# Kernel optimization log

Hardware: AMD Instinct MI355X
Metric: run time of the kernel (lower is better)

The kernel has to match this reference:

```python
import jax, jax.numpy as jnp
import numpy as np
from jax import lax

B, D, S, H, W, T = 128, 512, 30, 14, 14, 12


def setup_inputs() -> dict:
    key = jax.random.key(0)
    ks = jax.random.split(key, 28)
    f = lambda k, shape: jax.random.normal(k, shape, jnp.float32) * 0.05
    return {
        "q": f(ks[0], (B, D)),
        "cws": f(ks[1], (B, D, S)),
        "KB": f(ks[2], (B, D, H, W)),
        "c0": f(ks[3], (B, D)),
        "m0": f(ks[4], (B, D)),
        "Wq": f(ks[5], (D, D)), "bq": f(ks[6], (D,)),
        "Wct": f(ks[7], (2 * D, D)), "bct": f(ks[8], (D,)),
        "wca": f(ks[9], (D,)), "bca": f(ks[10], ()),
        "Wm": f(ks[11], (D, D)), "bm": f(ks[12], (D,)),
        "Wkb": f(ks[13], (D, D)), "bkb": f(ks[14], (D,)),
        "Wrm": f(ks[15], (2 * D, D)), "brm": f(ks[16], (D,)),
        "wra": f(ks[17], (D,)), "bra": f(ks[18], ()),
        "Wwm": f(ks[19], (2 * D, D)), "bwm": f(ks[20], (D,)),
        "wwa": f(ks[21], (D,)), "bwa": f(ks[22], ()),
        "Wam": f(ks[23], (2 * D, D)), "bam": f(ks[24], (D,)),
        "Wg": f(ks[25], (D, D)), "bg": f(ks[26], (D,)),
        "steps": T,
    }


def _mac(q, cws, KB, c0, m0, Wq, bq, Wct, bct, wca, bca, Wm, bm, Wkb, bkb,
         Wrm, brm, wra, bra, Wwm, bwm, wwa, bwa, Wam, bam, Wg, bg, steps):
    b, d, h, w = KB.shape[0], KB.shape[1], KB.shape[2], KB.shape[3]
    KBp = jnp.transpose(KB, (0, 2, 3, 1))          # B,H,W,d
    KB2 = KBp @ Wkb + bkb                           # KB_transform (step-invariant)
    q_i = q @ Wq + bq                               # q_transform (step-invariant)

    nhist = steps + 1
    c_hist = jnp.zeros((nhist, b, d), KB.dtype).at[0].set(c0)
    m_hist = jnp.zeros((nhist, b, d), KB.dtype).at[0].set(m0)

    def step(carry, t):
        c_hist, m_hist, c_prev, m_prev = carry
        # ---- ControlUnit ----
        cq = jnp.concatenate([q_i, c_prev], axis=-1) @ Wct + bct   # B,d
        clog = jnp.einsum('bds,d->bs', cq[:, :, None] * cws, wca) + bca
        cattn = jax.nn.softmax(clog, axis=-1)                       # B,S
        c_i = jnp.einsum('bs,bds->bd', cattn, cws)
        # ---- ReadUnit ----
        mp = m_prev @ Wm + bm                                       # B,d
        I = mp[:, None, None, :] * KB2                              # B,H,W,d
        Im = jnp.concatenate([I, KBp], axis=-1) @ Wrm + brm         # B,H,W,d
        rlog = jnp.einsum('bhwd,d->bhw', c_i[:, None, None, :] * Im, wra) + bra
        rattn = jax.nn.softmax(rlog.reshape(b, -1), axis=-1).reshape(b, h, w)
        m_new = jnp.einsum('bhw,bhwd->bd', rattn, KBp)
        # ---- WriteUnit (self_attn + mem_gate) ----
        _m = jnp.concatenate([m_new, m_prev], axis=-1) @ Wwm + bwm
        slog = jnp.einsum('tbd,d->bt', c_i[None] * c_hist, wwa) + bwa
        valid = jnp.arange(nhist) <= t
        slog = jnp.where(valid[None, :], slog, jnp.float32(-1e9))
        sattn = jax.nn.softmax(slog, axis=-1)                       # B,T+1
        m_sa = jnp.einsum('bt,tbd->bd', sattn, m_hist)
        _m = jnp.concatenate([m_sa, _m], axis=-1) @ Wam + bam
        g = jax.nn.sigmoid(c_i @ Wg + bg)
        _m = g * m_prev + (1.0 - g) * _m
        c_hist = c_hist.at[t + 1].set(c_i)
        m_hist = m_hist.at[t + 1].set(_m)
        return (c_hist, m_hist, c_i, _m), None

    (c_hist, m_hist, c_last, m_last), _ = lax.scan(
        step, (c_hist, m_hist, c0, m0), jnp.arange(steps))
    return m_last


def reference(q, cws, KB, c0, m0, Wq, bq, Wct, bct, wca, bca, Wm, bm, Wkb, bkb,
              Wrm, brm, wra, bra, Wwm, bwm, wwa, bwa, Wam, bam, Wg, bg, steps):
    return _mac(q, cws, KB, c0, m0, Wq, bq, Wct, bct, wca, bca, Wm, bm, Wkb, bkb,
                Wrm, brm, wra, bra, Wwm, bwm, wwa, bwa, Wam, bam, Wg, bg, steps)
```

## Files before the change

kernel.cpp:

```cpp
#include <hip/hip_runtime.h>
#include <cstdint>

#define BB 128
#define DD 512
#define SS 30
#define PP 196
#define TT 12
#define BD (BB*DD)

typedef unsigned short ushortT;
typedef unsigned int uintT;

__device__ __forceinline__ float bf2f(ushortT u)
{
    return __uint_as_float(((uintT)u) << 16);
}
__device__ __forceinline__ ushortT f2bf(float f)
{
    uintT b = __float_as_uint(f);
    return (ushortT)((b + 0x7FFFu + ((b >> 16) & 1u)) >> 16);
}

struct GDesc {
    const float *A0, *A1;
    const ushortT *W0, *W1;
    const float *bias;
    float *out;
    const float *e1;
    int nparts, epi, mblk, nblk, aux;
};
struct GPack { GDesc d[6]; };

__global__ __launch_bounds__(256)
void gemm4(GPack pk)
{
    GDesc d = pk.d[blockIdx.z];
    if ((int)blockIdx.x >= d.mblk || (int)blockIdx.y >= d.nblk) return;
    const int tid  = threadIdx.x;
    const int lane = tid & 63;
    const int wv   = __builtin_amdgcn_readfirstlane(tid >> 6);

    if (d.epi == 5) {
        int bb = (blockIdx.x * 4 + blockIdx.y) * 2;
        #pragma unroll
        for (int b = bb; b < bb + 2; ++b) {
            const float* sat = d.e1 + b * 16;
            float a0 = 0.f, a1 = 0.f;
            for (int tp = 0; tp <= d.aux; ++tp) {
                float s = sat[tp];
                const float* mh = d.A0 + (size_t)tp * BD + (size_t)b * DD;
                a0 = fmaf(s, mh[tid], a0);
                a1 = fmaf(s, mh[tid + 256], a1);
            }
            d.out[(size_t)b * DD + tid] = a0;
            d.out[(size_t)b * DD + tid + 256] = a1;
        }
        return;
    }

    const int m0 = blockIdx.x * 8;
    const int c0 = blockIdx.y * 128;
    float accx[8], accy[8];
    #pragma unroll
    for (int m = 0; m < 8; ++m) { accx[m] = 0.f; accy[m] = 0.f; }

    for (int p = 0; p < d.nparts; ++p) {
        const float* A = p ? d.A1 : d.A0;
        const ushortT* W = p ? d.W1 : d.W0;
        const float* a = A + (size_t)m0 * 512 + wv * 128;
        const uintT* Wb = (const uintT*)(W + (size_t)(wv * 128) * 512 + c0) + lane;
        #pragma unroll 4
        for (int k = 0; k < 128; ++k) {
            uintT w = Wb[(size_t)k * 256];
            float wx = __uint_as_float(w << 16);
            float wy = __uint_as_float(w & 0xFFFF0000u);
            #pragma unroll
            for (int m = 0; m < 8; ++m) {
                float av = a[m * 512 + k];
                accx[m] = fmaf(av, wx, accx[m]);
                accy[m] = fmaf(av, wy, accy[m]);
            }
        }
    }

    __shared__ float red[4][8][128];
    #pragma unroll
    for (int m = 0; m < 8; ++m)
        *(float2*)&red[wv][m][lane * 2] = make_float2(accx[m], accy[m]);
    __syncthreads();

    for (int i = tid; i < 1024; i += 256) {
        int mm = i >> 7, cl = i & 127;
        float s = (red[0][mm][cl] + red[1][mm][cl])
                + (red[2][mm][cl] + red[3][mm][cl]);
        int row = m0 + mm, col = c0 + cl;
        size_t o = (size_t)row * 512 + col;
        if (d.epi == 0)      d.out[o] = s + d.bias[col];
        else if (d.epi == 1) { float v = s + d.bias[col];
                               d.out[o] = 1.f / (1.f + __expf(-v)); }
        else if (d.epi == 4) d.out[o] = s + d.e1[o];
        else if (d.epi == 7) ((ushortT*)d.out)[o] = f2bf(s);
        else                 d.out[o] = s;
    }
}

struct SP {
    const float *cq, *cws, *wca, *bca, *wra, *wwa, *bwa;
    const ushortT *cwsTh;
    float *c_hist, *sattn, *vb;
    const float *msa, *mnw, *gb, *b2;
    const ushortT *WamH, *WAH, *WBH;
    float *m_hist, *dst;
    int t;
};

__global__ __launch_bounds__(512)
void stepA(SP P)
{
    const int tid = threadIdx.x;
    const int lane = tid & 63;
    __shared__ float cqw[512], ciw[512];
    __shared__ float clog2[32], cattn[32], slog[16];
    __shared__ float red[8][2][128];

    if ((int)blockIdx.x < 128) {
        if (P.t >= TT) return;
        int b = blockIdx.x, w = tid >> 6, t = P.t;
        cqw[tid] = P.cq[(size_t)b*DD + tid] * P.wca[tid];
        __syncthreads();
        for (int s = w; s < SS; s += 8) {
            const ushortT* row = P.cwsTh + ((size_t)b*SS + s)*DD;
            float a = 0.f;
            #pragma unroll
            for (int j = 0; j < 8; ++j)
                a = fmaf(cqw[lane + 64*j], bf2f(row[lane + 64*j]), a);
            for (int off = 32; off; off >>= 1) a += __shfl_xor(a, off, 64);
            if (lane == 0) clog2[s] = a;
        }
        __syncthreads();
        if (tid < 32) {
            float v = (tid < SS) ? clog2[tid] + P.bca[0] : -1e30f;
            float mx = v;
            for (int off = 16; off; off >>= 1) mx = fmaxf(mx, __shfl_xor(mx, off, 32));
            float e = (tid < SS) ? __expf(v - mx) : 0.f;
            float sm = e;
            for (int off = 16; off; off >>= 1) sm += __shfl_xor(sm, off, 32);
            cattn[tid] = e / sm;
        }
        __syncthreads();
        {
            const float* base = P.cws + (size_t)b*DD*SS + (size_t)tid*SS;
            float acc = 0.f;
            #pragma unroll
            for (int j = 0; j < SS; ++j) acc = fmaf(cattn[j], base[j], acc);
            P.c_hist[(size_t)(t+1)*BD + (size_t)b*DD + tid] = acc;
            P.vb[(size_t)b*DD + tid] = acc * P.wra[tid];
            ciw[tid] = acc * P.wwa[tid];
        }
        __syncthreads();
        for (int tp = tid >> 6; tp <= t; tp += 8) {
            const float* ch = P.c_hist + (size_t)tp*BD + (size_t)b*DD;
            float a = 0.f;
            #pragma unroll
            for (int j = 0; j < 8; ++j)
                a = fmaf(ciw[lane + 64*j], ch[lane + 64*j], a);
            for (int off = 32; off; off >>= 1) a += __shfl_xor(a, off, 64);
            if (lane == 0) slog[tp] = a;
        }
        __syncthreads();
        if (tid < 16) {
            float v = (tid <= t) ? slog[tid] + P.bwa[0] : -1e30f;
            float mx = v;
            for (int off = 8; off; off >>= 1) mx = fmaxf(mx, __shfl_xor(mx, off, 16));
            float e = (tid <= t) ? __expf(v - mx) : 0.f;
            float sm = e;
            for (int off = 8; off; off >>= 1) sm += __shfl_xor(sm, off, 16);
            P.sattn[b*16 + tid] = e / sm;
        }
    } else {
        if (P.t == 0) return;
        int gb_ = blockIdx.x - 128;
        int mt = gb_ >> 2, nc = gb_ & 3;
        int wv = __builtin_amdgcn_readfirstlane(tid >> 6);
        const int koff = wv * 64;
        const float* mprev = P.m_hist + (size_t)(P.t - 1) * BD;
        const int r0 = mt * 2;
        float ax0 = 0.f, ay0 = 0.f, ax1 = 0.f, ay1 = 0.f;

        const float* As[3] = { P.msa, P.mnw, mprev };
        const ushortT* Ws[3] = { P.WamH, P.WAH, P.WBH };
        #pragma unroll
        for (int seg = 0; seg < 3; ++seg) {
            const float* a = As[seg] + (size_t)r0 * 512 + koff;
            const uintT* Wb = (const uintT*)(Ws[seg] + (size_t)koff * 512 + nc * 128) + lane;
            #pragma unroll 8
            for (int k = 0; k < 64; ++k) {
                uintT w = Wb[(size_t)k * 256];
                float wx = __uint_as_float(w << 16);
                float wy = __uint_as_float(w & 0xFFFF0000u);
                float av0 = a[k], av1 = a[512 + k];
                ax0 = fmaf(av0, wx, ax0); ay0 = fmaf(av0, wy, ay0);
                ax1 = fmaf(av1, wx, ax1); ay1 = fmaf(av1, wy, ay1);
            }
        }
        *(float2*)&red[wv][0][lane*2] = make_float2(ax0, ay0);
        *(float2*)&red[wv][1][lane*2] = make_float2(ax1, ay1);
        __syncthreads();
        if (tid < 256) {
            int mm = tid >> 7, cl = tid & 127;
            float s = 0.f;
            #pragma unroll
            for (int j = 0; j < 8; ++j) s += red[j][mm][cl];
            int row = r0 + mm, col = nc*128 + cl;
            size_t o = (size_t)row*512 + col;
            float v = s + P.b2[col];
            float g = P.gb[o];
            float pv = mprev[o];
            P.dst[o] = g*pv + (1.f - g)*v;
        }
    }
}

__global__ __launch_bounds__(256)
void read1y(const ushortT* __restrict__ KBh, const float* __restrict__ ubuf,
            const float* __restrict__ mp, const float* __restrict__ WkbT,
            const float* __restrict__ vW, float* __restrict__ rlogp)
{
    int b = blockIdx.x, dg = blockIdx.y, tid = threadIdx.x;
    int lane = tid & 63, w = tid >> 6;
    __shared__ float red[4][64];
    __shared__ float yb[64];
    {
        const float* ur = ubuf + (size_t)b*512;
        const float* mr = mp + (size_t)b*512;
        const float* Wc = WkbT + dg*64 + lane;
        float s = 0.f;
        for (int k = w*128; k < w*128 + 128; ++k)
            s = fmaf(ur[k]*mr[k], Wc[(size_t)k*512], s);
        red[w][lane] = s;
    }
    __syncthreads();
    if (tid < 64)
        yb[tid] = (red[0][tid]+red[1][tid]) + (red[2][tid]+red[3][tid])
                + vW[(size_t)b*512 + dg*64 + tid];
    __syncthreads();
    float a0=0.f, a1=0.f, a2=0.f, a3=0.f;
    if (tid < PP) {
        const ushortT* kb = KBh + ((size_t)b*512 + dg*64)*PP + tid;
        #pragma unroll 4
        for (int dd = 0; dd < 64; dd += 4) {
            a0 = fmaf(bf2f(kb[(size_t)(dd+0)*PP]), yb[dd+0], a0);
            a1 = fmaf(bf2f(kb[(size_t)(dd+1)*PP]), yb[dd+1], a1);
            a2 = fmaf(bf2f(kb[(size_t)(dd+2)*PP]), yb[dd+2], a2);
            a3 = fmaf(bf2f(kb[(size_t)(dd+3)*PP]), yb[dd+3], a3);
        }
    }
    rlogp[((size_t)b*8 + dg)*256 + tid] = (a0+a1)+(a2+a3);
}

__global__ __launch_bounds__(256)
void read2(const ushortT* __restrict__ KBh, const float* __restrict__ rlogp,
           float* __restrict__ m_new)
{
    int b = blockIdx.x, dg = blockIdx.y;
    int tid = threadIdx.x, lane = tid & 63, w = tid >> 6;
    __shared__ float ex[256];
    __shared__ float wred[4];

    float v = -1e30f;
    if (tid < PP) {
        const float* rp = rlogp + (size_t)b*2048 + tid;
        float t0 = rp[0]    + rp[256];
        float t1 = rp[512]  + rp[768];
        float t2 = rp[1024] + rp[1280];
        float t3 = rp[1536] + rp[1792];
        v = (t0+t1)+(t2+t3);
    }
    float mx = v;
    for (int off = 32; off; off >>= 1) mx = fmaxf(mx, __shfl_xor(mx, off, 64));
    if (lane == 0) wred[w] = mx;
    __syncthreads();
    float gmax = fmaxf(fmaxf(wred[0], wred[1]), fmaxf(wred[2], wred[3]));
    float e = (tid < PP) ? __expf(v - gmax) : 0.f;
    float sm = e;
    for (int off = 32; off; off >>= 1) sm += __shfl_xor(sm, off, 64);
    __syncthreads();
    if (lane == 0) wred[w] = sm;
    __syncthreads();
    float inv = 1.f / ((wred[0]+wred[1]) + (wred[2]+wred[3]));
    ex[tid] = e * inv;
    __syncthreads();

    #pragma unroll 2
    for (int i = 0; i < 16; ++i) {
        int d = dg*64 + w*16 + i;
        const ushortT* row = KBh + ((size_t)b*512 + d)*PP;
        float a = ex[lane]       * bf2f(row[lane])
                + ex[lane + 64]  * bf2f(row[lane + 64])
                + ex[lane + 128] * bf2f(row[lane + 128]);
        if (lane < PP - 192) a = fmaf(ex[lane + 192], bf2f(row[lane + 192]), a);
        for (int off = 32; off; off >>= 1) a += __shfl_xor(a, off, 64);
        if (lane == 0) m_new[(size_t)b*512 + d] = a;
    }
}

struct SetupP {
    const float *Wrm, *Wkb, *cws, *KB, *c0v, *m0v, *bwm;
    const float *Wam, *Wam_bot, *bam, *Wg, *Wm, *Wq, *Wct;
    float *WkbT, *c_hist, *m_hist, *b2;
    ushortT *KBh, *cwsTh, *WamH, *WgH, *WmH, *WqH, *WambH, *WctHt, *WctHb;
    ushortT *WrmTuH, *WrmTvH;
};

__global__ __launch_bounds__(256)
void setup_misc(SetupP P)
{
    __shared__ float tile[32][33];
    int id = blockIdx.x, tid = threadIdx.x;

    if (id < 768) {
        int which = id >> 8, tj = id & 255;
        const float* src = (which == 0) ? P.Wrm
                         : (which == 1) ? (P.Wrm + 512*512) : P.Wkb;
        int bx = (tj & 15) * 32, by = (tj >> 4) * 32;
        int tx = tid & 31, ty = tid >> 5;
        #pragma unroll
        for (int i = 0; i < 32; i += 8)
            tile[ty+i][tx] = src[(size_t)(by+ty+i)*512 + bx+tx];
        __syncthreads();
        if (which == 2) {
            #pragma unroll
            for (int i = 0; i < 32; i += 8)
                P.WkbT[(size_t)(bx+ty+i)*512 + by+tx] = tile[tx][ty+i];
        } else {
            ushortT* dst = which ? P.WrmTvH : P.WrmTuH;
            #pragma unroll
            for (int i = 0; i < 32; i += 8)
                dst[(size_t)(bx+ty+i)*512 + by+tx] = f2bf(tile[tx][ty+i]);
        }
    } else if (id < 2816) {
        int j = id - 768;
        int b = j >> 4, dc = j & 15;
        const float* src = P.cws + ((size_t)b*DD + dc*32) * SS;
        for (int i = tid; i < 1024; i += 256) {
            int r = i >> 5, s = i & 31;
            if (s < SS) tile[r][s] = src[(size_t)r*SS + s];
        }
        __syncthreads();
        for (int i = tid; i < 1024; i += 256) {
            int s = i >> 5, r = i & 31;
            if (s < SS)
                P.cwsTh[((size_t)b*SS + s)*DD + dc*32 + r] = f2bf(tile[r][s]);
        }
    } else if (id < 9088) {
        size_t i = ((size_t)(id - 2816) * 256 + tid) * 8;
        #pragma unroll
        for (int j = 0; j < 8; ++j)
            P.KBh[i + j] = f2bf(P.KB[i + j]);
    } else if (id < 9344) {
        int i = (id - 9088) * 256 + tid;
        P.c_hist[i] = P.c0v[i];
        P.m_hist[i] = P.m0v[i];
    } else if (id < 9352) {
        int lane = tid & 63, w = tid >> 6;
        int n = (id - 9344) * 64 + lane;
        float s = 0.f;
        for (int k = w*128; k < w*128 + 128; ++k)
            s = fmaf(P.bwm[k], P.Wam_bot[(size_t)k*512 + n], s);
        __shared__ float red[4][64];
        red[w][lane] = s;
        __syncthreads();
        if (tid < 64) {
            int nn = (id - 9344) * 64 + tid;
            P.b2[nn] = red[0][tid] + red[1][tid] + red[2][tid] + red[3][tid]
                     + P.bam[nn];
        }
    } else {
        int j = id - 9352;
        int which = j >> 7, blk = j & 127;
        const float* src = (which == 0) ? P.Wam
                         : (which == 1) ? P.Wg
                         : (which == 2) ? P.Wm
                         : (which == 3) ? P.Wq
                         : (which == 4) ? P.Wam_bot
                         : (which == 5) ? P.Wct : (P.Wct + 512*512);
        ushortT* dst = (which == 0) ? P.WamH
                     : (which == 1) ? P.WgH
                     : (which == 2) ? P.WmH
                     : (which == 3) ? P.WqH
                     : (which == 4) ? P.WambH
                     : (which == 5) ? P.WctHt : P.WctHb;
        size_t i = ((size_t)blk * 256 + tid) * 8;
        #pragma unroll
        for (int jj = 0; jj < 8; ++jj)
            dst[i + jj] = f2bf(src[i + jj]);
    }
}

extern "C" void kernel_launch(void* const* d_in, const int* in_sizes, int n_in,
                              void* d_out, int out_size, void* d_ws, size_t ws_size,
                              hipStream_t stream)
{
    (void)in_sizes; (void)n_in; (void)out_size; (void)ws_size;
    const float* q   = (const float*)d_in[0];
    const float* cws = (const float*)d_in[1];
    const float* KB  = (const float*)d_in[2];
    const float* c0  = (const float*)d_in[3];
    const float* m0  = (const float*)d_in[4];
    const float* Wq  = (const float*)d_in[5];
    const float* bq  = (const float*)d_in[6];
    const float* Wct = (const float*)d_in[7];
    const float* bct = (const float*)d_in[8];
    const float* wca = (const float*)d_in[9];
    const float* bca = (const float*)d_in[10];
    const float* Wm  = (const float*)d_in[11];
    const float* bm  = (const float*)d_in[12];
    const float* Wkb = (const float*)d_in[13];
    const float* Wrm = (const float*)d_in[15];
    const float* wra = (const float*)d_in[17];
    const float* Wwm = (const float*)d_in[19];
    const float* bwm = (const float*)d_in[20];
    const float* wwa = (const float*)d_in[21];
    const float* bwa = (const float*)d_in[22];
    const float* Wam = (const float*)d_in[23];
    const float* bam = (const float*)d_in[24];
    const float* Wg  = (const float*)d_in[25];
    const float* bg  = (const float*)d_in[26];

    float* ws      = (float*)d_ws;
    float* c_hist  = ws;
    float* m_hist  = ws + 13*BD;
    float* qct     = ws + 26*BD;
    float* q_i     = ws + 27*BD;
    float* cq      = ws + 28*BD;
    float* mp      = ws + 29*BD;
    float* vb      = ws + 30*BD;
    float* ubuf    = ws + 31*BD;
    float* vW      = ws + 32*BD;
    float* gb      = ws + 33*BD;
    float* msa     = ws + 34*BD;
    float* mnw     = ws + 35*BD;
    float* sattn   = ws + 36*BD;
    float* rlogp   = ws + 37*BD;
    float* WkbT    = ws + 49*BD;
    float* b2      = ws + 61*BD;
    ushortT* cwsTh = (ushortT*)(ws + 62*BD);
    ushortT* KBh   = (ushortT*)(ws + 92*BD);
    ushortT* WamH  = (ushortT*)(ws + 190*BD);
    ushortT* WAH   = (ushortT*)(ws + 192*BD);
    ushortT* WBH   = (ushortT*)(ws + 194*BD);
    ushortT* WgH   = (ushortT*)(ws + 196*BD);
    ushortT* WmH   = (ushortT*)(ws + 198*BD);
    ushortT* WqH   = (ushortT*)(ws + 200*BD);
    ushortT* WambH = (ushortT*)(ws + 202*BD);
    ushortT* WctHt = (ushortT*)(ws + 204*BD);
    ushortT* WctHb = (ushortT*)(ws + 206*BD);
    ushortT* WrmTuH= (ushortT*)(ws + 208*BD);
    ushortT* WrmTvH= (ushortT*)(ws + 210*BD);

    const float* Wam_bot = Wam + 512*512;
    const float* Wwm_bot = Wwm + 512*512;
    dim3 blk(256);
    GDesc Z = { nullptr,nullptr,nullptr,nullptr,nullptr,nullptr,nullptr,
                1, 6, 0, 0, 0 };

    {
        SetupP S;
        S.Wrm = Wrm; S.Wkb = Wkb; S.cws = cws; S.KB = KB;
        S.c0v = c0; S.m0v = m0; S.bwm = bwm;
        S.Wam = Wam; S.Wam_bot = Wam_bot; S.bam = bam;
        S.Wg = Wg; S.Wm = Wm; S.Wq = Wq; S.Wct = Wct;
        S.WkbT = WkbT; S.c_hist = c_hist; S.m_hist = m_hist; S.b2 = b2;
        S.KBh = KBh; S.cwsTh = cwsTh;
        S.WamH = WamH; S.WgH = WgH; S.WmH = WmH; S.WqH = WqH;
        S.WambH = WambH; S.WctHt = WctHt; S.WctHb = WctHb;
        S.WrmTuH = WrmTuH; S.WrmTvH = WrmTvH;
        setup_misc<<<dim3(10248), blk, 0, stream>>>(S);
    }
    {
        GPack pk;
        pk.d[0] = { Wwm, nullptr, WambH, nullptr, nullptr, (float*)WAH,
                    nullptr, 1, 7, 64, 4, 0 };
        pk.d[1] = { Wwm_bot, nullptr, WambH, nullptr, nullptr, (float*)WBH,
                    nullptr, 1, 7, 64, 4, 0 };
        pk.d[2] = { q, nullptr, WqH, nullptr, bq, q_i, nullptr,
                    1, 0, 16, 4, 0 };
        pk.d[3] = Z; pk.d[4] = Z; pk.d[5] = Z;
        gemm4<<<dim3(64,4,3), blk, 0, stream>>>(pk);
    }
    {
        GPack pk;
        pk.d[0] = { q_i, nullptr, WctHt, nullptr, bct, qct, nullptr,
                    1, 0, 16, 4, 0 };
        pk.d[1] = { q_i, c0, WctHt, WctHb, bct, cq, nullptr,
                    2, 0, 16, 4, 0 };
        pk.d[2] = Z; pk.d[3] = Z; pk.d[4] = Z; pk.d[5] = Z;
        gemm4<<<dim3(16,4,2), blk, 0, stream>>>(pk);
    }

    for (int t = 0; t <= TT; ++t) {
        {
            SP P;
            P.cq = cq; P.cws = cws; P.cwsTh = cwsTh;
            P.wca = wca; P.bca = bca; P.wra = wra; P.wwa = wwa; P.bwa = bwa;
            P.c_hist = c_hist; P.sattn = sattn; P.vb = vb;
            P.msa = msa; P.mnw = mnw; P.gb = gb; P.b2 = b2;
            P.WamH = WamH; P.WAH = WAH; P.WBH = WBH;
            P.m_hist = m_hist;
            P.dst = (t == TT) ? (float*)d_out : (m_hist + (size_t)t * BD);
            P.t = t;
            stepA<<<dim3(384), dim3(512), 0, stream>>>(P);
        }
        if (t == TT) break;

        float* c_i = c_hist + (size_t)(t+1) * BD;
        {
            GPack pk;
            pk.d[0] = { vb, nullptr, WrmTuH, nullptr, nullptr, ubuf, nullptr,
                        1, 6, 16, 4, 0 };
            pk.d[1] = { vb, nullptr, WrmTvH, nullptr, nullptr, vW, nullptr,
                        1, 6, 16, 4, 0 };
            pk.d[2] = { c_i, nullptr, WgH, nullptr, bg, gb, nullptr,
                        1, 1, 16, 4, 0 };
            pk.d[3] = { c_i, nullptr, WctHb, nullptr, nullptr, cq, qct,
                        1, 4, 16, 4, 0 };
            pk.d[4] = { m_hist + (size_t)t * BD, nullptr, WmH, nullptr, bm, mp,
                        nullptr, 1, 0, 16, 4, 0 };
            pk.d[5] = { m_hist, nullptr, nullptr, nullptr, nullptr, msa, sattn,
                        1, 5, 16, 4, t };
            gemm4<<<dim3(16,4,6), blk, 0, stream>>>(pk);
        }
        read1y<<<dim3(BB,8), blk, 0, stream>>>(KBh, ubuf, mp, WkbT, vW, rlogp);
        read2<<<dim3(BB,8), blk, 0, stream>>>(KBh, rlogp, mnw);
    }
}
```

Measured before the change: 756.3 us.

## Use bf16 cws and Wkb copies, fold q_transform into setup kernel

Result: no change. 761.0 us (+0.6%).

```diff
diff --git a/kernel.cpp b/kernel.cpp
--- a/kernel.cpp
+++ b/kernel.cpp
@@ -105,7 +105,7 @@
 }
 
 struct SP {
-    const float *cq, *cws, *wca, *bca, *wra, *wwa, *bwa;
+    const float *cq, *wca, *bca, *wra, *wwa, *bwa;
     const ushortT *cwsTh;
     float *c_hist, *sattn, *vb;
     const float *msa, *mnw, *gb, *b2;
@@ -149,10 +149,11 @@
         }
         __syncthreads();
         {
-            const float* base = P.cws + (size_t)b*DD*SS + (size_t)tid*SS;
+            const ushortT* baseh = P.cwsTh + (size_t)b*SS*DD + tid;
             float acc = 0.f;
             #pragma unroll
-            for (int j = 0; j < SS; ++j) acc = fmaf(cattn[j], base[j], acc);
+            for (int j = 0; j < SS; ++j)
+                acc = fmaf(cattn[j], bf2f(baseh[(size_t)j*DD]), acc);
             P.c_hist[(size_t)(t+1)*BD + (size_t)b*DD + tid] = acc;
             P.vb[(size_t)b*DD + tid] = acc * P.wra[tid];
             ciw[tid] = acc * P.wwa[tid];
@@ -223,7 +224,7 @@
 
 __global__ __launch_bounds__(256)
 void read1y(const ushortT* __restrict__ KBh, const float* __restrict__ ubuf,
-            const float* __restrict__ mp, const float* __restrict__ WkbT,
+            const float* __restrict__ mp, const ushortT* __restrict__ WkbTh,
             const float* __restrict__ vW, float* __restrict__ rlogp)
 {
     int b = blockIdx.x, dg = blockIdx.y, tid = threadIdx.x;
@@ -233,10 +234,10 @@
     {
         const float* ur = ubuf + (size_t)b*512;
         const float* mr = mp + (size_t)b*512;
-        const float* Wc = WkbT + dg*64 + lane;
+        const ushortT* Wc = WkbTh + dg*64 + lane;
         float s = 0.f;
         for (int k = w*128; k < w*128 + 128; ++k)
-            s = fmaf(ur[k]*mr[k], Wc[(size_t)k*512], s);
+            s = fmaf(ur[k]*mr[k], bf2f(Wc[(size_t)k*512]), s);
         red[w][lane] = s;
     }
     __syncthreads();
@@ -306,10 +307,10 @@
 
 struct SetupP {
     const float *Wrm, *Wkb, *cws, *KB, *c0v, *m0v, *bwm;
-    const float *Wam, *Wam_bot, *bam, *Wg, *Wm, *Wq, *Wct;
-    float *WkbT, *c_hist, *m_hist, *b2;
+    const float *Wam, *Wam_bot, *bam, *Wg, *Wm, *Wq, *bq, *Wct, *q;
+    float *c_hist, *m_hist, *b2, *q_i;
     ushortT *KBh, *cwsTh, *WamH, *WgH, *WmH, *WqH, *WambH, *WctHt, *WctHb;
-    ushortT *WrmTuH, *WrmTvH;
+    ushortT *WrmTuH, *WrmTvH, *WkbTH;
 };
 
 __global__ __launch_bounds__(256)
@@ -322,22 +323,17 @@
         int which = id >> 8, tj = id & 255;
         const float* src = (which == 0) ? P.Wrm
                          : (which == 1) ? (P.Wrm + 512*512) : P.Wkb;
+        ushortT* dst = (which == 0) ? P.WrmTuH
+                     : (which == 1) ? P.WrmTvH : P.WkbTH;
         int bx = (tj & 15) * 32, by = (tj >> 4) * 32;
         int tx = tid & 31, ty = tid >> 5;
         #pragma unroll
         for (int i = 0; i < 32; i += 8)
             tile[ty+i][tx] = src[(size_t)(by+ty+i)*512 + bx+tx];
         __syncthreads();
-        if (which == 2) {
-            #pragma unroll
-            for (int i = 0; i < 32; i += 8)
-                P.WkbT[(size_t)(bx+ty+i)*512 + by+tx] = tile[tx][ty+i];
-        } else {
-            ushortT* dst = which ? P.WrmTvH : P.WrmTuH;
-            #pragma unroll
-            for (int i = 0; i < 32; i += 8)
-                dst[(size_t)(bx+ty+i)*512 + by+tx] = f2bf(tile[tx][ty+i]);
-        }
+        #pragma unroll
+        for (int i = 0; i < 32; i += 8)
+            dst[(size_t)(bx+ty+i)*512 + by+tx] = f2bf(tile[tx][ty+i]);
     } else if (id < 2816) {
         int j = id - 768;
         int b = j >> 4, dc = j & 15;
@@ -375,7 +371,7 @@
             P.b2[nn] = red[0][tid] + red[1][tid] + red[2][tid] + red[3][tid]
                      + P.bam[nn];
         }
-    } else {
+    } else if (id < 10248) {
         int j = id - 9352;
         int which = j >> 7, blk = j & 127;
         const float* src = (which == 0) ? P.Wam
@@ -394,6 +390,18 @@
         #pragma unroll
         for (int jj = 0; jj < 8; ++jj)
             dst[i + jj] = f2bf(src[i + jj]);
+    } else {
+        int r = id - 10248;
+        const float* qa = P.q + (size_t)r * 512;
+        float acc0 = 0.f, acc1 = 0.f;
+        #pragma unroll 4
+        for (int k = 0; k < 512; ++k) {
+            float av = qa[k];
+            acc0 = fmaf(av, P.Wq[(size_t)k*512 + tid], acc0);
+            acc1 = fmaf(av, P.Wq[(size_t)k*512 + tid + 256], acc1);
+        }
+        P.q_i[(size_t)r*512 + tid]       = acc0 + P.bq[tid];
+        P.q_i[(size_t)r*512 + tid + 256] = acc1 + P.bq[tid + 256];
     }
 }
 
@@ -442,7 +450,7 @@
     float* mnw     = ws + 35*BD;
     float* sattn   = ws + 36*BD;
     float* rlogp   = ws + 37*BD;
-    float* WkbT    = ws + 49*BD;
+    ushortT* WkbTH = (ushortT*)(ws + 49*BD);
     float* b2      = ws + 61*BD;
     ushortT* cwsTh = (ushortT*)(ws + 62*BD);
     ushortT* KBh   = (ushortT*)(ws + 92*BD);
@@ -469,13 +477,13 @@
         S.Wrm = Wrm; S.Wkb = Wkb; S.cws = cws; S.KB = KB;
         S.c0v = c0; S.m0v = m0; S.bwm = bwm;
         S.Wam = Wam; S.Wam_bot = Wam_bot; S.bam = bam;
-        S.Wg = Wg; S.Wm = Wm; S.Wq = Wq; S.Wct = Wct;
-        S.WkbT = WkbT; S.c_hist = c_hist; S.m_hist = m_hist; S.b2 = b2;
+        S.Wg = Wg; S.Wm = Wm; S.Wq = Wq; S.bq = bq; S.Wct = Wct; S.q = q;
+        S.c_hist = c_hist; S.m_hist = m_hist; S.b2 = b2; S.q_i = q_i;
         S.KBh = KBh; S.cwsTh = cwsTh;
         S.WamH = WamH; S.WgH = WgH; S.WmH = WmH; S.WqH = WqH;
         S.WambH = WambH; S.WctHt = WctHt; S.WctHb = WctHb;
-        S.WrmTuH = WrmTuH; S.WrmTvH = WrmTvH;
-        setup_misc<<<dim3(10248), blk, 0, stream>>>(S);
+        S.WrmTuH = WrmTuH; S.WrmTvH = WrmTvH; S.WkbTH = WkbTH;
+        setup_misc<<<dim3(10376), blk, 0, stream>>>(S);
     }
     {
         GPack pk;
@@ -483,25 +491,18 @@
                     nullptr, 1, 7, 64, 4, 0 };
         pk.d[1] = { Wwm_bot, nullptr, WambH, nullptr, nullptr, (float*)WBH,
                     nullptr, 1, 7, 64, 4, 0 };
-        pk.d[2] = { q, nullptr, WqH, nullptr, bq, q_i, nullptr,
+        pk.d[2] = { q_i, nullptr, WctHt, nullptr, bct, qct, nullptr,
                     1, 0, 16, 4, 0 };
-        pk.d[3] = Z; pk.d[4] = Z; pk.d[5] = Z;
-        gemm4<<<dim3(64,4,3), blk, 0, stream>>>(pk);
-    }
-    {
-        GPack pk;
-        pk.d[0] = { q_i, nullptr, WctHt, nullptr, bct, qct, nullptr,
-                    1, 0, 16, 4, 0 };
-        pk.d[1] = { q_i, c0, WctHt, WctHb, bct, cq, nullptr,
+        pk.d[3] = { q_i, c0, WctHt, WctHb, bct, cq, nullptr,
                     2, 0, 16, 4, 0 };
-        pk.d[2] = Z; pk.d[3] = Z; pk.d[4] = Z; pk.d[5] = Z;
-        gemm4<<<dim3(16,4,2), blk, 0, stream>>>(pk);
+        pk.d[4] = Z; pk.d[5] = Z;
+        gemm4<<<dim3(64,4,4), blk, 0, stream>>>(pk);
     }
 
     for (int t = 0; t <= TT; ++t) {
         {
             SP P;
-            P.cq = cq; P.cws = cws; P.cwsTh = cwsTh;
+            P.cq = cq; P.cwsTh = cwsTh;
             P.wca = wca; P.bca = bca; P.wra = wra; P.wwa = wwa; P.bwa = bwa;
             P.c_hist = c_hist; P.sattn = sattn; P.vb = vb;
             P.msa = msa; P.mnw = mnw; P.gb = gb; P.b2 = b2;
@@ -530,7 +531,7 @@
                         1, 5, 16, 4, t };
             gemm4<<<dim3(16,4,6), blk, 0, stream>>>(pk);
         }
-        read1y<<<dim3(BB,8), blk, 0, stream>>>(KBh, ubuf, mp, WkbT, vW, rlogp);
+        read1y<<<dim3(BB,8), blk, 0, stream>>>(KBh, ubuf, mp, WkbTH, vW, rlogp);
         read2<<<dim3(BB,8), blk, 0, stream>>>(KBh, rlogp, mnw);
     }
 }
```
